# Optimization experiments

Measured on AMD Instinct MI355X. Metric: run time of the kernel, lower is better.

Reference implementation:

```python
import jax, jax.numpy as jnp
import numpy as np

N_ENT = 100000
N_REL = 500
D = 50
N_EDGES = 2000000


def segment_softmax(scores, seg, n):
    # numerically stable softmax over edges grouped by segment id
    m = jax.ops.segment_max(scores, seg, num_segments=n)
    m = jnp.where(jnp.isfinite(m), m, 0.0)
    e = jnp.exp(scores - m[seg])
    s = jax.ops.segment_sum(e, seg, num_segments=n)
    return e / (s[seg] + 1e-9)


def kbgat(h, r, t, E, R, W, a, Wr, relation_relu, n_ent):
    # relation transform
    rel = R @ Wr
    if relation_relu:
        rel = jax.nn.relu(rel)
    d = E.shape[1]
    # per-triple feature: concat(E[h], R[r], E[t]) @ W, computed without materializing the concat
    feat = E[h] @ W[:d] + R[r] @ W[d:2 * d] + E[t] @ W[2 * d:]  # [n_edges, units]
    score = jax.nn.leaky_relu(feat @ a, 0.2)                      # [n_edges]
    alpha = segment_softmax(score, h, n_ent)                      # softmax over neighbors of each head entity
    out = jax.ops.segment_sum(alpha[:, None] * feat, h, num_segments=n_ent)  # [n_ent, units]
    return out, rel


def setup_inputs() -> dict:
    key = jax.random.key(0)
    ks = jax.random.split(key, 14)
    std = np.sqrt(1.0 / D).astype(np.float32)
    h_index = jax.random.randint(ks[0], (N_EDGES,), 0, N_ENT, dtype=jnp.int32)
    r_index = jax.random.randint(ks[1], (N_EDGES,), 0, N_REL, dtype=jnp.int32)
    t_index = jax.random.randint(ks[2], (N_EDGES,), 0, N_ENT, dtype=jnp.int32)
    E = jax.random.normal(ks[3], (N_ENT, D), dtype=jnp.float32) * std
    R = jax.random.normal(ks[4], (N_REL, D), dtype=jnp.float32) * std
    g = lambda k, shape, fan: jax.random.normal(k, shape, dtype=jnp.float32) * np.sqrt(1.0 / fan).astype(np.float32)
    W0 = g(ks[5], (3 * D, D), 3 * D)
    a0 = g(ks[6], (D,), D)
    Wr0 = g(ks[7], (D, D), D)
    W1 = g(ks[8], (3 * D, D), 3 * D)
    a1 = g(ks[9], (D,), D)
    Wr1 = g(ks[10], (D, D), D)
    Wd = g(ks[11], (D, D), D)
    bd = jnp.zeros((D,), dtype=jnp.float32)
    return {"h_index": h_index, "r_index": r_index, "t_index": t_index,
            "E": E, "R": R, "W0": W0, "a0": a0, "Wr0": Wr0,
            "W1": W1, "a1": a1, "Wr1": Wr1, "Wd": Wd, "bd": bd}


def reference(h_index, r_index, t_index, E, R, W0, a0, Wr0, W1, a1, Wr1, Wd, bd):
    # dropout rate = 0 -> identity. num_heads = 1 -> concat / add_n are identities.
    e0, rel0 = kbgat(h_index, r_index, t_index, E, R, W0, a0, Wr0, True, N_ENT)
    e1, rel1 = kbgat(h_index, r_index, t_index, e0, rel0, W1, a1, Wr1, False, N_ENT)
    entity_features = e1 + E @ Wd + bd  # residual dense on original entity embeddings
    return entity_features, rel1
```

## Files before the change

### kernel.cpp

```cpp
#include <hip/hip_runtime.h>

#define N_ENT   100000
#define N_REL   500
#define DD      50
#define LD      52
#define LD2     64
#define LDH     64
#define N_EDGES 2000000
#define T_BITS  17
#define T_MASK  0x1FFFF
#define BBITS   9
#define BMASK   511
#define NB      196
#define CHUNK   4096
#define ENT_BLOCKS   2500
#define BKT_BLOCKS   489
#define HIST_BLOCKS  1024
#define REL_BLOCKS   100

typedef float v2f __attribute__((ext_vector_type(2)));

__device__ inline unsigned int pack_bf2(float x, float y) {
    unsigned int xu = __float_as_uint(x);
    unsigned int yu = __float_as_uint(y);
    xu = (xu + 0x7FFFu + ((xu >> 16) & 1u)) >> 16;
    yu = (yu + 0x7FFFu + ((yu >> 16) & 1u)) >> 16;
    return xu | (yu << 16);
}
__device__ inline v2f unpk2(unsigned int v) {
    v2f r;
    r.x = __uint_as_float(v << 16);
    r.y = __uint_as_float(v & 0xFFFF0000u);
    return r;
}

template<int NMAT>
__device__ void ent_pre_body(float* smemF, int bid,
    const float* __restrict__ X, int ldX,
    const float* __restrict__ Wa,
    const float* __restrict__ Wb,
    const float* __restrict__ Wc,
    const float* __restrict__ bd,
    const float* __restrict__ avec,
    float* __restrict__ Ya,
    unsigned short* __restrict__ Ybh,
    float* __restrict__ Yc,
    float* __restrict__ shOut,
    float* __restrict__ stOut)
{
    constexpr int MT = 40;
    float* sW = smemF;
    float* sX = sW + NMAT * DD * DD;
    float* sY = sX + MT * 52;
    float* sa = sY + MT * 52;

    const int tid = threadIdx.x;

    for (int i = tid; i < DD * DD / 4; i += 512) {
        ((float4*)sW)[i] = ((const float4*)Wa)[i];
        ((float4*)(sW + DD * DD))[i] = ((const float4*)Wb)[i];
        if (NMAT == 3) ((float4*)(sW + 2 * DD * DD))[i] = ((const float4*)Wc)[i];
    }
    if (tid < DD) sa[tid] = avec[tid];

    const int m0 = bid * MT;
    const int nX4 = MT * ldX / 4;
    const float4* xsrc = (const float4*)(X + (size_t)m0 * ldX);
    for (int i = tid; i < nX4; i += 512) ((float4*)sX)[i] = xsrc[i];
    __syncthreads();

    const bool active = (tid < 500);
    const int mp = active ? tid / 25 : 0;
    const int jp = active ? tid % 25 : 0;
    const int r0 = 2 * mp, r1 = 2 * mp + 1, j0 = 2 * jp;

    float acc[NMAT][2][2];
    #pragma unroll
    for (int t = 0; t < NMAT; t++)
        #pragma unroll
        for (int i = 0; i < 2; i++)
            #pragma unroll
            for (int c = 0; c < 2; c++) acc[t][i][c] = 0.f;

    if (active) {
        if (NMAT == 3) {
            float b0 = bd[j0], b1 = bd[j0 + 1];
            acc[2][0][0] = b0; acc[2][0][1] = b1;
            acc[2][1][0] = b0; acc[2][1][1] = b1;
        }
        const float* xr0 = &sX[r0 * ldX];
        const float* xr1 = &sX[r1 * ldX];
        for (int k = 0; k < DD; k++) {
            float x0 = xr0[k], x1 = xr1[k];
            #pragma unroll
            for (int t = 0; t < NMAT; t++) {
                float2 w = *(const float2*)&sW[t * DD * DD + k * DD + j0];
                acc[t][0][0] += x0 * w.x; acc[t][0][1] += x0 * w.y;
                acc[t][1][0] += x1 * w.x; acc[t][1][1] += x1 * w.y;
            }
        }
    }

    if (tid < MT * 2) sY[(tid >> 1) * 52 + 50 + (tid & 1)] = 0.f;

    if (active) {
        sY[r0 * 52 + j0]     = acc[0][0][0];
        sY[r0 * 52 + j0 + 1] = acc[0][0][1];
        sY[r1 * 52 + j0]     = acc[0][1][0];
        sY[r1 * 52 + j0 + 1] = acc[0][1][1];
    }
    __syncthreads();
    {
        float4* dst = (float4*)(Ya + (size_t)m0 * LD);
        for (int i = tid; i < MT * LD / 4; i += 512) dst[i] = ((const float4*)sY)[i];
        if (tid < MT) {
            const float* row = &sY[tid * 52];
            float d = 0.f;
            for (int k = 0; k < DD; k++) d += row[k] * sa[k];
            shOut[m0 + tid] = d;
        }
    }
    __syncthreads();

    unsigned int* sYhU = (unsigned int*)sX;
    if (active) {
        sY[r0 * 52 + j0]     = acc[1][0][0];
        sY[r0 * 52 + j0 + 1] = acc[1][0][1];
        sY[r1 * 52 + j0]     = acc[1][1][0];
        sY[r1 * 52 + j0 + 1] = acc[1][1][1];
        sYhU[r0 * 32 + jp] = pack_bf2(acc[1][0][0], acc[1][0][1]);
        sYhU[r1 * 32 + jp] = pack_bf2(acc[1][1][0], acc[1][1][1]);
    }
    if (tid < MT * 7) sYhU[(tid / 7) * 32 + 25 + (tid % 7)] = 0u;
    __syncthreads();
    {
        float4* dst = (float4*)(Ybh + (size_t)m0 * LDH);
        for (int i = tid; i < MT * LDH * 2 / 16; i += 512) dst[i] = ((const float4*)sYhU)[i];
        if (tid < MT) {
            const float* row = &sY[tid * 52];
            float d = 0.f;
            for (int k = 0; k < DD; k++) d += row[k] * sa[k];
            stOut[m0 + tid] = d;
        }
    }

    if (NMAT == 3) {
        __syncthreads();
        if (active) {
            sY[r0 * 52 + j0]     = acc[2][0][0];
            sY[r0 * 52 + j0 + 1] = acc[2][0][1];
            sY[r1 * 52 + j0]     = acc[2][1][0];
            sY[r1 * 52 + j0 + 1] = acc[2][1][1];
        }
        __syncthreads();
        float4* dst = (float4*)(Yc + (size_t)m0 * LD);
        for (int i = tid; i < MT * LD / 4; i += 512) dst[i] = ((const float4*)sY)[i];
    }
}

template<int NMAT>
__global__ __launch_bounds__(512) void ent_pre_v6(
    const float* __restrict__ X, int ldX,
    const float* __restrict__ Wa,
    const float* __restrict__ Wb,
    const float* __restrict__ Wc,
    const float* __restrict__ bd,
    const float* __restrict__ avec,
    float* __restrict__ Ya,
    unsigned short* __restrict__ Ybh,
    float* __restrict__ Yc,
    float* __restrict__ shOut,
    float* __restrict__ stOut)
{
    __shared__ __align__(16) float smemF[NMAT * DD * DD + 40 * 52 * 2 + 64];
    ent_pre_body<NMAT>(smemF, blockIdx.x, X, ldX, Wa, Wb, Wc, bd, avec,
                       Ya, Ybh, Yc, shOut, stOut);
}

__device__ void rel_body(float* smemF, int bid,
    const float* __restrict__ Rin, int ld_in,
    const float* __restrict__ Wr,
    const float* __restrict__ Wmid,
    const float* __restrict__ avec,
    int do_relu,
    float* __restrict__ rel_out, int ld_rel,
    float* __restrict__ RW_out,
    float* __restrict__ sr)
{
    float* sWr  = smemF;
    float* sWm  = sWr + DD * DD;
    float* sRed = sWm + DD * DD;

    for (int i = threadIdx.x; i < DD * DD; i += blockDim.x) {
        sWr[i] = Wr[i];
        sWm[i] = Wmid[i];
    }
    __syncthreads();
    const int tid = threadIdx.x;
    const bool act = (tid < 250);
    const int m = bid * 5 + tid / 50;
    const int j = tid % 50;
    float am = 0.f;
    if (act) {
        const float* x = Rin + (size_t)m * ld_in;
        float ar = 0.f;
        for (int k = 0; k < DD; k++) {
            float xv = x[k];
            ar += xv * sWr[k * DD + j];
            am += xv * sWm[k * DD + j];
        }
        if (do_relu) ar = fmaxf(ar, 0.f);
        rel_out[(size_t)m * ld_rel + j] = ar;
        RW_out[(size_t)m * LD2 + j] = am;
        if (j < LD2 - DD) RW_out[(size_t)m * LD2 + DD + j] = 0.f;
    }
    if (tid < 256) sRed[tid] = act ? am * avec[j] : 0.f;
    __syncthreads();
    if (tid < 5) {
        float d = 0.f;
        const float* p = &sRed[tid * 50];
        for (int k = 0; k < 50; k++) d += p[k];
        sr[bid * 5 + tid] = d;
    }
}


__device__ void coarse_hist_body(int* sH, int bid,
    const int* __restrict__ h, int* __restrict__ ccoarse, int nE4)
{
    for (int i = threadIdx.x; i < NB; i += 256) sH[i] = 0;
    __syncthreads();
    const int stride = HIST_BLOCKS * 256;
    const int4* h4 = (const int4*)h;
    for (int i = bid * 256 + threadIdx.x; i < nE4; i += stride) {
        int4 v = h4[i];
        atomicAdd(&sH[v.x >> BBITS], 1);
        atomicAdd(&sH[v.y >> BBITS], 1);
        atomicAdd(&sH[v.z >> BBITS], 1);
        atomicAdd(&sH[v.w >> BBITS], 1);
    }
    __syncthreads();
    for (int i = threadIdx.x; i < NB; i += 256) {
        int v = sH[i];
        if (v) atomicAdd(&ccoarse[i], v);
    }
}

__global__ __launch_bounds__(256) void hist_rel0_kernel(
    const int* __restrict__ h, int* __restrict__ ccoarse, int nE4,
    const float* __restrict__ Rin,
    const float* __restrict__ Wr,
    const float* __restrict__ Wmid,
    const float* __restrict__ avec,
    float* __restrict__ rel_out,
    float* __restrict__ RW_out,
    float* __restrict__ sr)
{
    __shared__ __align__(16) float smemF[2 * DD * DD + 256 + 16];
    if (blockIdx.x < REL_BLOCKS) {
        rel_body(smemF, blockIdx.x, Rin, DD, Wr, Wmid, avec, 1,
                 rel_out, LD, RW_out, sr);
    } else {
        coarse_hist_body((int*)smemF, blockIdx.x - REL_BLOCKS, h, ccoarse, nE4);
    }
}

__global__ void coarse_scan_kernel(const int* __restrict__ ccoarse,
                                   int* __restrict__ cbase,
                                   int* __restrict__ ccur)
{
    __shared__ int s[256];
    const int b = threadIdx.x;
    int sum = (b < NB) ? ccoarse[b] : 0;
    s[b] = sum;
    __syncthreads();
    for (int off = 1; off < 256; off <<= 1) {
        int v = (b >= off) ? s[b - off] : 0;
        __syncthreads();
        s[b] += v;
        __syncthreads();
    }
    if (b < NB) {
        int excl = s[b] - sum;
        cbase[b] = excl;
        ccur[b] = excl;
    }
    if (b == NB - 1) cbase[NB] = s[b];
}

__device__ void bucket_body(float* smemF, int bid,
    const int* __restrict__ h,
    const int* __restrict__ r,
    const int* __restrict__ t,
    int* __restrict__ ccur,
    unsigned int* __restrict__ stagedP,
    unsigned short* __restrict__ stagedH, int nE)
{
    int* sHist = (int*)smemF;
    int* sScan = sHist + NB;
    int* sBase = sScan + 512;
    int* sCur  = sBase + NB;
    int* sGb   = sCur + NB;
    unsigned int*   sPay = (unsigned int*)(sGb + NB);
    unsigned short* sLoc = (unsigned short*)(sPay + CHUNK);
    unsigned char*  sBkt = (unsigned char*)(sLoc + CHUNK);

    const int tid = threadIdx.x;
    const int e0 = bid * CHUNK;
    const int n = min(CHUNK, nE - e0);

    for (int i = tid; i < NB; i += 512) sHist[i] = 0;
    __syncthreads();

    #pragma unroll
    for (int k = 0; k < CHUNK / 512; k++) {
        int e = e0 + k * 512 + tid;
        if (e < nE) atomicAdd(&sHist[h[e] >> BBITS], 1);
    }
    __syncthreads();

    int v = (tid < NB) ? sHist[tid] : 0;
    sScan[tid] = v;
    __syncthreads();
    for (int off = 1; off < 512; off <<= 1) {
        int x = (tid >= off) ? sScan[tid - off] : 0;
        __syncthreads();
        sScan[tid] += x;
        __syncthreads();
    }
    if (tid < NB) {
        int excl = sScan[tid] - v;
        sBase[tid] = excl;
        sCur[tid] = excl;
    }
    __syncthreads();

    #pragma unroll
    for (int k = 0; k < CHUNK / 512; k++) {
        int e = e0 + k * 512 + tid;
        if (e < nE) {
            int hv = h[e];
            int b = hv >> BBITS;
            int pos = atomicAdd(&sCur[b], 1);
            sPay[pos] = ((unsigned int)r[e] << T_BITS) | (unsigned int)t[e];
            sLoc[pos] = (unsigned short)(hv & BMASK);
            sBkt[pos] = (unsigned char)b;
        }
    }
    __syncthreads();

    if (tid < NB) {
        int cnt = sHist[tid];
        sGb[tid] = cnt ? atomicAdd(&ccur[tid], cnt) : 0;
    }
    __syncthreads();

    for (int i = tid; i < n; i += 512) {
        int b = sBkt[i];
        int g = sGb[b] + (i - sBase[b]);
        stagedP[g] = sPay[i];
        stagedH[g] = sLoc[i];
    }
}

__global__ __launch_bounds__(512) void fused0_kernel(
    const float* __restrict__ E,
    const float* __restrict__ W0,
    const float* __restrict__ Wd,
    const float* __restrict__ bd,
    const float* __restrict__ a0,
    float* __restrict__ EW1,
    unsigned short* __restrict__ EW3h,
    float* __restrict__ Ed,
    float* __restrict__ sh,
    float* __restrict__ st,
    const int* __restrict__ h,
    const int* __restrict__ r,
    const int* __restrict__ t,
    int* __restrict__ ccur,
    unsigned int* __restrict__ stagedP,
    unsigned short* __restrict__ stagedH, int nE)
{
    __shared__ __align__(16) float smemF[3 * DD * DD + 40 * 52 * 2 + 64];
    if (blockIdx.x < BKT_BLOCKS) {
        bucket_body(smemF, blockIdx.x, h, r, t, ccur, stagedP, stagedH, nE);
    } else {
        ent_pre_body<3>(smemF, blockIdx.x - BKT_BLOCKS, E, DD,
                        W0, W0 + 2 * DD * DD, Wd, bd, a0,
                        EW1, EW3h, Ed, sh, st);
    }
}

__device__ void final_scatter_body(float* smemF, int b,
    const unsigned int* __restrict__ stagedP,
    const unsigned short* __restrict__ stagedH,
    const int* __restrict__ cbase,
    int* __restrict__ counts,
    int* __restrict__ s0,
    unsigned int* __restrict__ rtp)
{
    int* sCnt  = (int*)smemF;
    int* sScan = sCnt + 512;
    int* sOff  = sScan + 512;

    const int i0 = cbase[b], i1 = cbase[b + 1];
    const int tid = threadIdx.x;

    sCnt[tid] = 0;
    __syncthreads();

    for (int i = i0 + tid; i < i1; i += 512)
        atomicAdd(&sCnt[stagedH[i]], 1);
    __syncthreads();

    const int v = sCnt[tid];
    sScan[tid] = v;
    __syncthreads();
    for (int off = 1; off < 512; off <<= 1) {
        int x = (tid >= off) ? sScan[tid - off] : 0;
        __syncthreads();
        sScan[tid] += x;
        __syncthreads();
    }
    const int excl = sScan[tid] - v;
    sOff[tid] = excl;

    const int u = (b << BBITS) + tid;
    if (u < N_ENT) {
        counts[u] = v;
        s0[u] = i0 + excl;
    }
    __syncthreads();

    for (int i = i0 + tid; i < i1; i += 512) {
        unsigned int p = stagedP[i];
        int loc = stagedH[i];
        int pos = i0 + atomicAdd(&sOff[loc], 1);
        rtp[pos] = p;
    }
}

__global__ __launch_bounds__(512) void fs_rel1_kernel(
    const unsigned int* __restrict__ stagedP,
    const unsigned short* __restrict__ stagedH,
    const int* __restrict__ cbase,
    int* __restrict__ counts,
    int* __restrict__ s0,
    unsigned int* __restrict__ rtp,
    const float* __restrict__ rel0,
    const float* __restrict__ Wr1,
    const float* __restrict__ Wmid1,
    const float* __restrict__ a1,
    float* __restrict__ out_rel,
    float* __restrict__ RW1,
    float* __restrict__ sr1)
{
    __shared__ __align__(16) float smemF[2 * DD * DD + 256 + 1600];
    if (blockIdx.x < NB) {
        final_scatter_body(smemF, blockIdx.x, stagedP, stagedH, cbase,
                           counts, s0, rtp);
    } else {
        rel_body(smemF, blockIdx.x - NB, rel0, LD, Wr1, Wmid1, a1, 0,
                 out_rel, DD, RW1, sr1);
    }
}

__global__ __launch_bounds__(256) void accum_fused_kernel(
    const int* __restrict__ s0v,
    const int* __restrict__ counts,
    const unsigned int* __restrict__ rtp,
    const float* __restrict__ sh,
    const float* __restrict__ sr,
    const float* __restrict__ st,
    const float* __restrict__ EW1,
    const float* __restrict__ RW,
    const unsigned short* __restrict__ EW3h,
    const float* __restrict__ base,
    float* __restrict__ outp, int full_ld)
{
    const int wid = (blockIdx.x * blockDim.x + threadIdx.x) >> 6;
    if (2 * wid >= N_ENT) return;
    const int lane  = threadIdx.x & 63;
    const int half  = lane >> 5;
    const int hlane = lane & 31;
    const int eg = hlane >> 3;
    const int q  = hlane & 7;
    const int sbase = half << 5;
    const unsigned qh = (unsigned)q << 4;
    const unsigned qr = (unsigned)q << 5;

    const int u = 2 * wid + half;
    const int b = s0v[u];
    const int c = counts[u];
    const float shu = sh[u];

    const char* __restrict__ pH = (const char*)EW3h;
    const char* __restrict__ pR = (const char*)RW;
    const char* __restrict__ pS = (const char*)sr;
    const char* __restrict__ pT = (const char*)st;

    v2f acc2[4];
    #pragma unroll
    for (int k = 0; k < 4; k++) { acc2[k].x = 0.f; acc2[k].y = 0.f; }
    float asum = 0.f;

    for (int i0 = 0; i0 < c; i0 += 32) {
        const int cb = min(32, c - i0);
        const int e = i0 + hlane;
        const unsigned w = rtp[b + min(e, c - 1)];
        float ex = 0.f;
        if (e < c) {
            float srv = *(const float*)(pS + ((w >> T_BITS) << 2));
            float stv = *(const float*)(pT + ((w & T_MASK) << 2));
            float sc = shu + srv + stv;
            sc = sc >= 0.f ? sc : 0.2f * sc;
            ex = __expf(sc);
        }
        asum += ex;

        const int nst = (cb + 3) >> 2;

#define LOADSTEP(S, TH, VA, VB, EX) {                                   \
        const int _src = sbase + min((S) * 4 + eg, cb - 1);             \
        const unsigned _wv = (unsigned)__shfl((int)w, _src);            \
        EX = __shfl(ex, _src);                                          \
        const unsigned _oH = ((_wv & T_MASK) << 7) | qh;                \
        const unsigned _oR = ((_wv >> T_BITS) << 8) | qr;               \
        TH = *(const uint4*)(pH + _oH);                                 \
        VA = *(const float4*)(pR + _oR);                                \
        VB = *(const float4*)(pR + _oR + 16); }

        uint4 th0, th1; float4 va0, vb0, va1, vb1; float ex0, ex1;
        LOADSTEP(0, th0, va0, vb0, ex0)
        LOADSTEP(1, th1, va1, vb1, ex1)

        for (int s = 0; s < nst; s++) {
            uint4 thn; float4 van, vbn; float exn;
            LOADSTEP(s + 2, thn, van, vbn, exn)

            const float exv = (s * 4 + eg < cb) ? ex0 : 0.f;
            v2f ex2; ex2.x = exv; ex2.y = exv;
            v2f p01; p01.x = va0.x; p01.y = va0.y;
            v2f p23; p23.x = va0.z; p23.y = va0.w;
            v2f p45; p45.x = vb0.x; p45.y = vb0.y;
            v2f p67; p67.x = vb0.z; p67.y = vb0.w;
            acc2[0] += ex2 * (p01 + unpk2(th0.x));
            acc2[1] += ex2 * (p23 + unpk2(th0.y));
            acc2[2] += ex2 * (p45 + unpk2(th0.z));
            acc2[3] += ex2 * (p67 + unpk2(th0.w));

            th0 = th1; va0 = va1; vb0 = vb1; ex0 = ex1;
            th1 = thn; va1 = van; vb1 = vbn; ex1 = exn;
        }
#undef LOADSTEP
    }

    const int ej = 8 * hlane;
    const bool ep = (hlane < 8) && (ej < LD);
    const bool efull = ep && (ej < 48);
    float4 w1a, w1b, ba, bb;
    if (ep) {
        const float* e1 = EW1 + (size_t)u * LD + (efull ? ej : 48);
        w1a = *(const float4*)e1;
        if (efull) w1b = *(const float4*)(e1 + 4);
        if (base) {
            const float* bp = base + (size_t)u * LD + (efull ? ej : 48);
            ba = *(const float4*)bp;
            if (efull) bb = *(const float4*)(bp + 4);
        }
    }

    float acc[8];
    #pragma unroll
    for (int k = 0; k < 4; k++) { acc[2 * k] = acc2[k].x; acc[2 * k + 1] = acc2[k].y; }
    #pragma unroll
    for (int off = 16; off >= 8; off >>= 1) {
        #pragma unroll
        for (int k = 0; k < 8; k++) acc[k] += __shfl_down(acc[k], off, 32);
        asum += __shfl_down(asum, off, 32);
    }
    asum += __shfl_xor(asum, 4);
    asum += __shfl_xor(asum, 2);
    asum += __shfl_xor(asum, 1);

    if (hlane >= 8) return;
    const int j0 = 8 * hlane;
    if (j0 >= LD) return;

    if (asum > 0.f) {
        float inv = 1.f / asum;
        if (j0 < 48) {
            acc[0] = w1a.x + acc[0] * inv; acc[1] = w1a.y + acc[1] * inv;
            acc[2] = w1a.z + acc[2] * inv; acc[3] = w1a.w + acc[3] * inv;
            acc[4] = w1b.x + acc[4] * inv; acc[5] = w1b.y + acc[5] * inv;
            acc[6] = w1b.z + acc[6] * inv; acc[7] = w1b.w + acc[7] * inv;
        } else {
            acc[0] = w1a.x + acc[0] * inv; acc[1] = w1a.y + acc[1] * inv;
            acc[2] = w1a.z + acc[2] * inv; acc[3] = w1a.w + acc[3] * inv;
        }
    }
    if (base) {
        if (j0 < 48) {
            acc[0] += ba.x; acc[1] += ba.y; acc[2] += ba.z; acc[3] += ba.w;
            acc[4] += bb.x; acc[5] += bb.y; acc[6] += bb.z; acc[7] += bb.w;
        } else {
            acc[0] += ba.x; acc[1] += ba.y; acc[2] += ba.z; acc[3] += ba.w;
        }
    }
    if (full_ld) {
        if (j0 < 48) {
            *(float4*)(outp + (size_t)u * LD + j0) =
                make_float4(acc[0], acc[1], acc[2], acc[3]);
            *(float4*)(outp + (size_t)u * LD + j0 + 4) =
                make_float4(acc[4], acc[5], acc[6], acc[7]);
        } else {
            *(float4*)(outp + (size_t)u * LD + 48) =
                make_float4(acc[0], acc[1], acc[2], acc[3]);
        }
    } else {
        float* row = outp + (size_t)u * DD;
        if (j0 < 48) {
            *(float2*)(row + j0)     = make_float2(acc[0], acc[1]);
            *(float2*)(row + j0 + 2) = make_float2(acc[2], acc[3]);
            *(float2*)(row + j0 + 4) = make_float2(acc[4], acc[5]);
            *(float2*)(row + j0 + 6) = make_float2(acc[6], acc[7]);
        } else {
            *(float2*)(row + 48) = make_float2(acc[0], acc[1]);
        }
    }
}

extern "C" void kernel_launch(void* const* d_in, const int* in_sizes, int n_in,
                              void* d_out, int out_size, void* d_ws, size_t ws_size,
                              hipStream_t stream)
{
    const int*   h   = (const int*)d_in[0];
    const int*   r   = (const int*)d_in[1];
    const int*   t   = (const int*)d_in[2];
    const float* E   = (const float*)d_in[3];
    const float* R   = (const float*)d_in[4];
    const float* W0  = (const float*)d_in[5];
    const float* a0  = (const float*)d_in[6];
    const float* Wr0 = (const float*)d_in[7];
    const float* W1  = (const float*)d_in[8];
    const float* a1  = (const float*)d_in[9];
    const float* Wr1 = (const float*)d_in[10];
    const float* Wd  = (const float*)d_in[11];
    const float* bd  = (const float*)d_in[12];

    float* out_ent = (float*)d_out;
    float* out_rel = out_ent + (size_t)N_ENT * DD;

    float* ws_f  = (float*)d_ws;
    float* EW1   = ws_f;
    float* Ed    = EW1  + (size_t)N_ENT * LD;
    float* e0    = Ed   + (size_t)N_ENT * LD;
    unsigned short* EW3h = (unsigned short*)(e0 + (size_t)N_ENT * LD);
    float* RW    = (float*)(EW3h + (size_t)N_ENT * LDH);
    float* RW1   = RW   + (size_t)N_REL * LD2;
    float* rel0  = RW1  + (size_t)N_REL * LD2;
    float* sh    = rel0 + (size_t)N_REL * LD;
    float* st    = sh   + N_ENT;
    float* sr    = st   + N_ENT;
    float* sr1   = sr   + N_REL;
    int* counts  = (int*)(sr1 + N_REL);
    int* s0      = counts + N_ENT;
    int* cbase   = s0 + N_ENT;
    int* ccur    = cbase + NB + 1;
    int* ccoarse = ccur + NB;
    unsigned int* rtp    = (unsigned int*)(ccoarse + NB);
    unsigned int*   stagedP = (unsigned int*)e0;
    unsigned short* stagedH = (unsigned short*)(e0 + (size_t)N_EDGES);

    const int BLK = 256;
    const int gW  = (N_ENT / 2 + 3) / 4;

    hipMemsetAsync(ccoarse, 0, (size_t)NB * sizeof(int), stream);
    hist_rel0_kernel<<<REL_BLOCKS + HIST_BLOCKS, BLK, 0, stream>>>(
        h, ccoarse, N_EDGES / 4, R, Wr0, W0 + DD * DD, a0, rel0, RW, sr);
    coarse_scan_kernel<<<1, 256, 0, stream>>>(ccoarse, cbase, ccur);

    fused0_kernel<<<BKT_BLOCKS + ENT_BLOCKS, 512, 0, stream>>>(
        E, W0, Wd, bd, a0, EW1, EW3h, Ed, sh, st,
        h, r, t, ccur, stagedP, stagedH, N_EDGES);

    fs_rel1_kernel<<<NB + REL_BLOCKS, 512, 0, stream>>>(
        stagedP, stagedH, cbase, counts, s0, rtp,
        rel0, Wr1, W1 + DD * DD, a1, out_rel, RW1, sr1);

    accum_fused_kernel<<<gW, BLK, 0, stream>>>(s0, counts, rtp, sh, sr, st,
                                               EW1, RW, EW3h, nullptr, e0, 1);

    ent_pre_v6<2><<<ENT_BLOCKS, 512, 0, stream>>>(e0, LD, W1, W1 + 2 * DD * DD,
                                                  nullptr, nullptr, a1,
                                                  EW1, EW3h, nullptr, sh, st);

    accum_fused_kernel<<<gW, BLK, 0, stream>>>(s0, counts, rtp, sh, sr1, st,
                                               EW1, RW1, EW3h, Ed, out_ent, 0);
}
```

Measured before the change: 381.7 us.

## Fuse layer-1 entity projection into layer-0 aggregation epilogue

Removes the separate ent_pre_v6<2> kernel. The first accumulation kernel now computes the layer-1 projections (EW1, bf16 EW3) and attention dot products directly from the aggregated rows held in shared memory. This avoids writing e0 to global memory and reading it back, and drops one launch. It adds per-block loading of two weight matrices, a scalar shared-memory matmul and shared atomics to every accumulation block. The intermediate buffers are rearranged: EW3 and the score arrays are double-buffered, and the staging buffers are moved off e0.

```diff
diff --git a/kernel.cpp b/kernel.cpp
--- a/kernel.cpp
+++ b/kernel.cpp
@@ -34,8 +34,7 @@
     return r;
 }
 
-template<int NMAT>
-__device__ void ent_pre_body(float* smemF, int bid,
+__device__ void ent_pre_body3(float* smemF, int bid,
     const float* __restrict__ X, int ldX,
     const float* __restrict__ Wa,
     const float* __restrict__ Wb,
@@ -48,6 +47,7 @@
     float* __restrict__ shOut,
     float* __restrict__ stOut)
 {
+    constexpr int NMAT = 3;
     constexpr int MT = 40;
     float* sW = smemF;
     float* sX = sW + NMAT * DD * DD;
@@ -59,7 +59,7 @@
     for (int i = tid; i < DD * DD / 4; i += 512) {
         ((float4*)sW)[i] = ((const float4*)Wa)[i];
         ((float4*)(sW + DD * DD))[i] = ((const float4*)Wb)[i];
-        if (NMAT == 3) ((float4*)(sW + 2 * DD * DD))[i] = ((const float4*)Wc)[i];
+        ((float4*)(sW + 2 * DD * DD))[i] = ((const float4*)Wc)[i];
     }
     if (tid < DD) sa[tid] = avec[tid];
 
@@ -83,11 +83,9 @@
             for (int c = 0; c < 2; c++) acc[t][i][c] = 0.f;
 
     if (active) {
-        if (NMAT == 3) {
-            float b0 = bd[j0], b1 = bd[j0 + 1];
-            acc[2][0][0] = b0; acc[2][0][1] = b1;
-            acc[2][1][0] = b0; acc[2][1][1] = b1;
-        }
+        float b0 = bd[j0], b1 = bd[j0 + 1];
+        acc[2][0][0] = b0; acc[2][0][1] = b1;
+        acc[2][1][0] = b0; acc[2][1][1] = b1;
         const float* xr0 = &sX[r0 * ldX];
         const float* xr1 = &sX[r1 * ldX];
         for (int k = 0; k < DD; k++) {
@@ -144,37 +142,16 @@
         }
     }
 
-    if (NMAT == 3) {
-        __syncthreads();
-        if (active) {
-            sY[r0 * 52 + j0]     = acc[2][0][0];
-            sY[r0 * 52 + j0 + 1] = acc[2][0][1];
-            sY[r1 * 52 + j0]     = acc[2][1][0];
-            sY[r1 * 52 + j0 + 1] = acc[2][1][1];
-        }
-        __syncthreads();
-        float4* dst = (float4*)(Yc + (size_t)m0 * LD);
-        for (int i = tid; i < MT * LD / 4; i += 512) dst[i] = ((const float4*)sY)[i];
-    }
-}
-
-template<int NMAT>
-__global__ __launch_bounds__(512) void ent_pre_v6(
-    const float* __restrict__ X, int ldX,
-    const float* __restrict__ Wa,
-    const float* __restrict__ Wb,
-    const float* __restrict__ Wc,
-    const float* __restrict__ bd,
-    const float* __restrict__ avec,
-    float* __restrict__ Ya,
-    unsigned short* __restrict__ Ybh,
-    float* __restrict__ Yc,
-    float* __restrict__ shOut,
-    float* __restrict__ stOut)
-{
-    __shared__ __align__(16) float smemF[NMAT * DD * DD + 40 * 52 * 2 + 64];
-    ent_pre_body<NMAT>(smemF, blockIdx.x, X, ldX, Wa, Wb, Wc, bd, avec,
-                       Ya, Ybh, Yc, shOut, stOut);
+    __syncthreads();
+    if (active) {
+        sY[r0 * 52 + j0]     = acc[2][0][0];
+        sY[r0 * 52 + j0 + 1] = acc[2][0][1];
+        sY[r1 * 52 + j0]     = acc[2][1][0];
+        sY[r1 * 52 + j0 + 1] = acc[2][1][1];
+    }
+    __syncthreads();
+    float4* dst = (float4*)(Yc + (size_t)m0 * LD);
+    for (int i = tid; i < MT * LD / 4; i += 512) dst[i] = ((const float4*)sY)[i];
 }
 
 __device__ void rel_body(float* smemF, int bid,
@@ -223,7 +200,6 @@
         sr[bid * 5 + tid] = d;
     }
 }
-
 
 __device__ void coarse_hist_body(int* sH, int bid,
     const int* __restrict__ h, int* __restrict__ ccoarse, int nE4)
@@ -385,9 +361,9 @@
     if (blockIdx.x < BKT_BLOCKS) {
         bucket_body(smemF, blockIdx.x, h, r, t, ccur, stagedP, stagedH, nE);
     } else {
-        ent_pre_body<3>(smemF, blockIdx.x - BKT_BLOCKS, E, DD,
-                        W0, W0 + 2 * DD * DD, Wd, bd, a0,
-                        EW1, EW3h, Ed, sh, st);
+        ent_pre_body3(smemF, blockIdx.x - BKT_BLOCKS, E, DD,
+                      W0, W0 + 2 * DD * DD, Wd, bd, a0,
+                      EW1, EW3h, Ed, sh, st);
     }
 }
 
@@ -465,6 +441,7 @@
     }
 }
 
+template<int FUSE>
 __global__ __launch_bounds__(256) void accum_fused_kernel(
     const int* __restrict__ s0v,
     const int* __restrict__ counts,
@@ -476,10 +453,29 @@
     const float* __restrict__ RW,
     const unsigned short* __restrict__ EW3h,
     const float* __restrict__ base,
-    float* __restrict__ outp, int full_ld)
-{
+    float* __restrict__ outp,
+    const float* __restrict__ Wga,
+    const float* __restrict__ Wgb,
+    const float* __restrict__ avec2,
+    float* __restrict__ EW1out,
+    unsigned short* __restrict__ EW3out,
+    float* __restrict__ sh1,
+    float* __restrict__ st1)
+{
+    constexpr int SWA = 0, SWB = 2512, SA = 5024, SROW = 5080,
+                  SYB = 5496, SDOTA = 5912, SDOTB = 5920, SMEMSZ = 5928;
+    __shared__ __align__(16) float smem[FUSE ? SMEMSZ : 4];
+
+    if constexpr (FUSE) {
+        for (int i = threadIdx.x; i < DD * DD / 4; i += 256) {
+            ((float4*)&smem[SWA])[i] = ((const float4*)Wga)[i];
+            ((float4*)&smem[SWB])[i] = ((const float4*)Wgb)[i];
+        }
+        if (threadIdx.x < DD) smem[SA + threadIdx.x] = avec2[threadIdx.x];
+        if (threadIdx.x < 16) smem[SDOTA + threadIdx.x] = 0.f;
+    }
+
     const int wid = (blockIdx.x * blockDim.x + threadIdx.x) >> 6;
-    if (2 * wid >= N_ENT) return;
     const int lane  = threadIdx.x & 63;
     const int half  = lane >> 5;
     const int hlane = lane & 31;
@@ -583,41 +579,31 @@
     asum += __shfl_xor(asum, 2);
     asum += __shfl_xor(asum, 1);
 
-    if (hlane >= 8) return;
-    const int j0 = 8 * hlane;
-    if (j0 >= LD) return;
-
-    if (asum > 0.f) {
-        float inv = 1.f / asum;
-        if (j0 < 48) {
-            acc[0] = w1a.x + acc[0] * inv; acc[1] = w1a.y + acc[1] * inv;
-            acc[2] = w1a.z + acc[2] * inv; acc[3] = w1a.w + acc[3] * inv;
-            acc[4] = w1b.x + acc[4] * inv; acc[5] = w1b.y + acc[5] * inv;
-            acc[6] = w1b.z + acc[6] * inv; acc[7] = w1b.w + acc[7] * inv;
-        } else {
-            acc[0] = w1a.x + acc[0] * inv; acc[1] = w1a.y + acc[1] * inv;
-            acc[2] = w1a.z + acc[2] * inv; acc[3] = w1a.w + acc[3] * inv;
-        }
-    }
-    if (base) {
-        if (j0 < 48) {
-            acc[0] += ba.x; acc[1] += ba.y; acc[2] += ba.z; acc[3] += ba.w;
-            acc[4] += bb.x; acc[5] += bb.y; acc[6] += bb.z; acc[7] += bb.w;
-        } else {
-            acc[0] += ba.x; acc[1] += ba.y; acc[2] += ba.z; acc[3] += ba.w;
-        }
-    }
-    if (full_ld) {
-        if (j0 < 48) {
-            *(float4*)(outp + (size_t)u * LD + j0) =
-                make_float4(acc[0], acc[1], acc[2], acc[3]);
-            *(float4*)(outp + (size_t)u * LD + j0 + 4) =
-                make_float4(acc[4], acc[5], acc[6], acc[7]);
-        } else {
-            *(float4*)(outp + (size_t)u * LD + 48) =
-                make_float4(acc[0], acc[1], acc[2], acc[3]);
-        }
-    } else {
+    if constexpr (!FUSE) {
+        if (hlane >= 8) return;
+        const int j0 = 8 * hlane;
+        if (j0 >= LD) return;
+
+        if (asum > 0.f) {
+            float inv = 1.f / asum;
+            if (j0 < 48) {
+                acc[0] = w1a.x + acc[0] * inv; acc[1] = w1a.y + acc[1] * inv;
+                acc[2] = w1a.z + acc[2] * inv; acc[3] = w1a.w + acc[3] * inv;
+                acc[4] = w1b.x + acc[4] * inv; acc[5] = w1b.y + acc[5] * inv;
+                acc[6] = w1b.z + acc[6] * inv; acc[7] = w1b.w + acc[7] * inv;
+            } else {
+                acc[0] = w1a.x + acc[0] * inv; acc[1] = w1a.y + acc[1] * inv;
+                acc[2] = w1a.z + acc[2] * inv; acc[3] = w1a.w + acc[3] * inv;
+            }
+        }
+        if (base) {
+            if (j0 < 48) {
+                acc[0] += ba.x; acc[1] += ba.y; acc[2] += ba.z; acc[3] += ba.w;
+                acc[4] += bb.x; acc[5] += bb.y; acc[6] += bb.z; acc[7] += bb.w;
+            } else {
+                acc[0] += ba.x; acc[1] += ba.y; acc[2] += ba.z; acc[3] += ba.w;
+            }
+        }
         float* row = outp + (size_t)u * DD;
         if (j0 < 48) {
             *(float2*)(row + j0)     = make_float2(acc[0], acc[1]);
@@ -626,6 +612,69 @@
             *(float2*)(row + j0 + 6) = make_float2(acc[6], acc[7]);
         } else {
             *(float2*)(row + 48) = make_float2(acc[0], acc[1]);
+        }
+    } else {
+        const int mloc = threadIdx.x >> 5;
+        const int j0 = 8 * hlane;
+        if (hlane < 7) {
+            float* rowp = &smem[SROW + mloc * 52];
+            if (asum > 0.f) {
+                float inv = 1.f / asum;
+                if (j0 < 48) {
+                    rowp[j0+0] = w1a.x + acc[0]*inv; rowp[j0+1] = w1a.y + acc[1]*inv;
+                    rowp[j0+2] = w1a.z + acc[2]*inv; rowp[j0+3] = w1a.w + acc[3]*inv;
+                    rowp[j0+4] = w1b.x + acc[4]*inv; rowp[j0+5] = w1b.y + acc[5]*inv;
+                    rowp[j0+6] = w1b.z + acc[6]*inv; rowp[j0+7] = w1b.w + acc[7]*inv;
+                } else {
+                    rowp[48] = w1a.x + acc[0]*inv; rowp[49] = w1a.y + acc[1]*inv;
+                    rowp[50] = 0.f; rowp[51] = 0.f;
+                }
+            } else {
+                if (j0 < 48) {
+                    #pragma unroll
+                    for (int k = 0; k < 8; k++) rowp[j0 + k] = 0.f;
+                } else {
+                    rowp[48] = 0.f; rowp[49] = 0.f; rowp[50] = 0.f; rowp[51] = 0.f;
+                }
+            }
+        }
+        __syncthreads();
+
+        const int u0 = blockIdx.x * 8;
+        for (int o = threadIdx.x; o < 416; o += 256) {
+            if (o < 400) {
+                const int m = o / 50, j = o - 50 * m;
+                const float* row = &smem[SROW + m * 52];
+                const float* wa = &smem[SWA + j];
+                const float* wb = &smem[SWB + j];
+                float dA = 0.f, dB = 0.f;
+                for (int k = 0; k < 50; k++) {
+                    float rv = row[k];
+                    dA += rv * wa[k * 50];
+                    dB += rv * wb[k * 50];
+                }
+                EW1out[(size_t)(u0 + m) * LD + j] = dA;
+                smem[SYB + m * 52 + j] = dB;
+                float av = smem[SA + j];
+                atomicAdd(&smem[SDOTA + m], dA * av);
+                atomicAdd(&smem[SDOTB + m], dB * av);
+            } else {
+                const int p = o - 400;
+                EW1out[(size_t)(u0 + (p >> 1)) * LD + 50 + (p & 1)] = 0.f;
+            }
+        }
+        __syncthreads();
+
+        {
+            const int m = threadIdx.x >> 5, jp = threadIdx.x & 31;
+            unsigned int val = 0u;
+            if (jp < 25) val = pack_bf2(smem[SYB + m * 52 + 2 * jp],
+                                        smem[SYB + m * 52 + 2 * jp + 1]);
+            ((unsigned int*)EW3out)[(size_t)(u0 + m) * 32 + jp] = val;
+            if (threadIdx.x < 8) {
+                sh1[u0 + threadIdx.x] = smem[SDOTA + threadIdx.x];
+                st1[u0 + threadIdx.x] = smem[SDOTB + threadIdx.x];
+            }
         }
     }
 }
@@ -654,26 +703,28 @@
     float* ws_f  = (float*)d_ws;
     float* EW1   = ws_f;
     float* Ed    = EW1  + (size_t)N_ENT * LD;
-    float* e0    = Ed   + (size_t)N_ENT * LD;
-    unsigned short* EW3h = (unsigned short*)(e0 + (size_t)N_ENT * LD);
-    float* RW    = (float*)(EW3h + (size_t)N_ENT * LDH);
+    unsigned short* EW3h  = (unsigned short*)(Ed + (size_t)N_ENT * LD);
+    unsigned short* EW3hb = EW3h + (size_t)N_ENT * LDH;
+    float* RW    = (float*)(EW3hb + (size_t)N_ENT * LDH);
     float* RW1   = RW   + (size_t)N_REL * LD2;
     float* rel0  = RW1  + (size_t)N_REL * LD2;
     float* sh    = rel0 + (size_t)N_REL * LD;
     float* st    = sh   + N_ENT;
-    float* sr    = st   + N_ENT;
+    float* sh1   = st   + N_ENT;
+    float* st1   = sh1  + N_ENT;
+    float* sr    = st1  + N_ENT;
     float* sr1   = sr   + N_REL;
     int* counts  = (int*)(sr1 + N_REL);
     int* s0      = counts + N_ENT;
     int* cbase   = s0 + N_ENT;
     int* ccur    = cbase + NB + 1;
     int* ccoarse = ccur + NB;
-    unsigned int* rtp    = (unsigned int*)(ccoarse + NB);
-    unsigned int*   stagedP = (unsigned int*)e0;
-    unsigned short* stagedH = (unsigned short*)(e0 + (size_t)N_EDGES);
+    unsigned int* rtp     = (unsigned int*)(ccoarse + NB);
+    unsigned int* stagedP = rtp + N_EDGES;
+    unsigned short* stagedH = (unsigned short*)(stagedP + N_EDGES);
 
     const int BLK = 256;
-    const int gW  = (N_ENT / 2 + 3) / 4;
+    const int gW  = N_ENT / 8;
 
     hipMemsetAsync(ccoarse, 0, (size_t)NB * sizeof(int), stream);
     hist_rel0_kernel<<<REL_BLOCKS + HIST_BLOCKS, BLK, 0, stream>>>(
@@ -688,13 +739,11 @@
         stagedP, stagedH, cbase, counts, s0, rtp,
         rel0, Wr1, W1 + DD * DD, a1, out_rel, RW1, sr1);
 
-    accum_fused_kernel<<<gW, BLK, 0, stream>>>(s0, counts, rtp, sh, sr, st,
-                                               EW1, RW, EW3h, nullptr, e0, 1);
-
-    ent_pre_v6<2><<<ENT_BLOCKS, 512, 0, stream>>>(e0, LD, W1, W1 + 2 * DD * DD,
-                                                  nullptr, nullptr, a1,
-                                                  EW1, EW3h, nullptr, sh, st);
-
-    accum_fused_kernel<<<gW, BLK, 0, stream>>>(s0, counts, rtp, sh, sr1, st,
-                                               EW1, RW1, EW3h, Ed, out_ent, 0);
-}
+    accum_fused_kernel<1><<<gW, BLK, 0, stream>>>(
+        s0, counts, rtp, sh, sr, st, EW1, RW, EW3h, nullptr, nullptr,
+        W1, W1 + 2 * DD * DD, a1, EW1, EW3hb, sh1, st1);
+
+    accum_fused_kernel<0><<<gW, BLK, 0, stream>>>(
+        s0, counts, rtp, sh1, sr1, st1, EW1, RW1, EW3hb, Ed, out_ent,
+        nullptr, nullptr, nullptr, nullptr, nullptr, nullptr, nullptr);
+}
```

Measured after the change: 436.4 us. 1.14x slower.
